# Optimization experiments

Measured on AMD Instinct MI355X. Metric: run time of the kernel, lower is better.

The kernel has to match this reference:

```python
import jax, jax.numpy as jnp
import numpy as np

# Intrinsics from innerProdLoss defaults
FX, FY, CX, CY = 48.0, 48.0, 48.0, 36.0
H, W = int(2 * CY), int(2 * CX)  # 72, 96
N = H * W                         # 6912 pixels
SIGMA2 = 1.0                      # geometric Gaussian-kernel bandwidth (reconstructed kern_mat)
EPS = 1e-8


def make_yz1_grid():
    # K = [[cx,fx,0],[cy,0,fy],[1,0,0]]; yz1_grid = inv(K) @ uv1_grid, shape [3, N]
    K = np.array([[CX, FX, 0.0], [CY, 0.0, FY], [1.0, 0.0, 0.0]], dtype=np.float64)
    invK = np.linalg.inv(K).astype(np.float32)
    u = np.arange(W, dtype=np.float32)
    v = np.arange(H, dtype=np.float32)
    uu = np.tile(u[None, :], (H, 1)).reshape(-1)
    vv = np.tile(v[:, None], (1, W)).reshape(-1)
    uv1 = np.stack([uu, vv, np.ones_like(uu)], axis=0)  # [3, N]
    return jnp.asarray(invK @ uv1)

YZ1 = make_yz1_grid()  # [3, N]


def kern_mat(p1, p2):
    # p1, p2: [B, 3, N] point clouds -> [B, N, N] Gaussian kernel exp(-||d||^2 / (2 sigma^2)).
    # Squared distances via norms + cross term (no [B,3,N,N] diff tensor).
    n1 = jnp.sum(p1 * p1, axis=1)                    # [B, N]
    n2 = jnp.sum(p2 * p2, axis=1)                    # [B, N]
    cross = jnp.einsum('bcm,bcn->bmn', p1, p2)       # [B, N, N]
    d2 = jnp.maximum(n1[:, :, None] + n2[:, None, :] - 2.0 * cross, 0.0)
    return jnp.exp(-d2 / (2.0 * SIGMA2))


def gramian(f1, f2):
    # f1, f2: [B, C, H, W] -> gramian [B, N, N] of L2-normalized features (norm_mode=1, kernalize=False).
    B, C, Hh, Ww = f1.shape
    n = Hh * Ww
    f1 = f1.reshape(B, C, n)
    f2 = f2.reshape(B, C, n)
    norm1 = jnp.linalg.norm(f1, axis=1)              # [B, N]
    norm2 = jnp.linalg.norm(f2, axis=1)
    fea_norm_sum = jnp.sum(norm1) + jnp.sum(norm2)
    f1n = f1 / (norm1[:, None, :] + EPS)
    f2n = f2 / (norm2[:, None, :] + EPS)
    gram = jnp.einsum('bcm,bcn->bmn', f1n, f2n) / n  # norm_mode=1 normalization
    return gram, fea_norm_sum


def setup_inputs() -> dict:
    key = jax.random.key(0)
    k1, k2, k3, k4, k5 = jax.random.split(key, 5)
    B, C = 1, 16
    feature1 = jax.random.normal(k1, (B, C, H, W), jnp.float32)
    feature2 = jax.random.normal(k2, (B, C, H, W), jnp.float32)
    depth1 = jax.random.uniform(k3, (B, 1, H, W), jnp.float32, 0.5, 5.0)
    depth2 = jax.random.uniform(k4, (B, 1, H, W), jnp.float32, 0.5, 5.0)
    pose1_2 = jnp.tile(jnp.eye(4, dtype=jnp.float32)[None], (B, 1, 1))
    pose_noise = jnp.eye(4, dtype=jnp.float32) + 0.01 * jax.random.normal(k5, (4, 4), jnp.float32)
    return {"feature1": feature1, "feature2": feature2, "depth1": depth1,
            "depth2": depth2, "pose1_2": pose1_2, "pose_noise": pose_noise}


def reference(feature1, feature2, depth1, depth2, pose1_2, pose_noise):
    B = depth1.shape[0]
    # gen_3D: back-project pixels using depth
    xyz1 = YZ1[None] * depth1.reshape(B, 1, N)       # [B, 3, N]
    xyz2 = YZ1[None] * depth2.reshape(B, 1, N)
    xyz2_homo = jnp.concatenate([xyz2, jnp.ones((B, 1, N), xyz2.dtype)], axis=1)  # [B, 4, N]
    xyz2_trans = jnp.matmul(pose1_2, xyz2_homo)[:, :3, :]

    gram_feat, fea_norm_sum = gramian(feature1, feature2)
    pcl_diff_exp = kern_mat(xyz1, xyz2_trans)

    # L2_norm=True, diff_mode=True -> scale by 100
    fea_norm_sum = fea_norm_sum * 100.0

    # diff_mode: noisy pose branch
    pose_noisy = jnp.matmul(pose1_2, pose_noise)
    xyz2_trans_noisy = jnp.matmul(pose_noisy, xyz2_homo)[:, :3, :]
    pcl_diff_exp_noisy = kern_mat(xyz1, xyz2_trans_noisy)

    inner_neg = -jnp.sum((pcl_diff_exp - pcl_diff_exp_noisy) * gram_feat)
    final_loss = inner_neg  # sparse_mode=False
    return final_loss, inner_neg, fea_norm_sum
```

## Files before the change

kernel.cpp:

```cpp
#include <hip/hip_runtime.h>
#include <math.h>

#define NPIX 6912
#define LOG2E 1.4426950408889634f

typedef __fp16 v8h  __attribute__((ext_vector_type(8)));
typedef float  v16f __attribute__((ext_vector_type(16)));

#define OFF_ROWFEAT 0
#define OFF_ROWGEO  221184
#define OFF_COLFEAT 442368
#define OFF_COLB1   663552
#define OFF_COLB2   884736
#define OFF_PART    1105920
#define OFF_NPART   1111104
#define NPART_BLOCKS 1296
#define NNORM_BLOCKS 108

__device__ __forceinline__ float fast_exp2(float x) { return __builtin_amdgcn_exp2f(x); }

__device__ __forceinline__ float wave_reduce_64(float v) {
    #pragma unroll
    for (int o = 32; o > 0; o >>= 1) v += __shfl_down(v, o, 64);
    return v;
}

__device__ __forceinline__ float block_reduce_256(float v, float* smem4) {
    __syncthreads();
    v = wave_reduce_64(v);
    const int lane = threadIdx.x & 63;
    const int w = threadIdx.x >> 6;
    if (lane == 0) smem4[w] = v;
    __syncthreads();
    float r = 0.0f;
    if (threadIdx.x == 0) r = smem4[0] + smem4[1] + smem4[2] + smem4[3];
    return r;
}

__device__ __forceinline__ void split_hl(float x, __fp16& h, __fp16& l) {
    h = (__fp16)x;
    l = (__fp16)(x - (float)h);
}

__global__ __launch_bounds__(64)
void preproc_kernel(const float* __restrict__ f1, const float* __restrict__ f2,
                    const float* __restrict__ d1, const float* __restrict__ d2,
                    const float* __restrict__ pose, const float* __restrict__ pnz,
                    char* __restrict__ wsb) {
    const int i = blockIdx.x * 64 + threadIdx.x;

    __fp16* rowfeat = (__fp16*)(wsb + OFF_ROWFEAT);
    __fp16* rowgeo  = (__fp16*)(wsb + OFF_ROWGEO);
    __fp16* colfeat = (__fp16*)(wsb + OFF_COLFEAT);
    __fp16* colB1   = (__fp16*)(wsb + OFF_COLB1);
    __fp16* colB2   = (__fp16*)(wsb + OFF_COLB2);
    float*  npart   = (float*)(wsb + OFF_NPART);

    float P[12];
    #pragma unroll
    for (int k = 0; k < 12; k++) P[k] = pose[k];
    float Q[12];
    #pragma unroll
    for (int r = 0; r < 3; r++) {
        #pragma unroll
        for (int c = 0; c < 4; c++) {
            float s = 0.0f;
            #pragma unroll
            for (int k = 0; k < 4; k++) s = fmaf(pose[r * 4 + k], pnz[k * 4 + c], s);
            Q[r * 4 + c] = s;
        }
    }

    const float inv48 = 1.0f / 48.0f;
    const int u = i % 96;
    const int v = i / 96;
    const float y1 = fmaf((float)u, inv48, -1.0f);
    const float y2 = fmaf((float)v, inv48, -0.75f);

    const float dep1 = d1[i];
    const float px = dep1, py = y1 * dep1, pz = y2 * dep1;
    const float n1 = px * px + py * py + pz * pz;
    const float wlog = -0.5f * LOG2E * n1;

    const float ptx = LOG2E * px, pty = LOG2E * py, ptz = LOG2E * pz;
    __fp16 phx, phy, phz, plx, ply, plz, wh, wl;
    split_hl(ptx, phx, plx);
    split_hl(pty, phy, ply);
    split_hl(ptz, phz, plz);
    split_hl(wlog, wh, wl);
    {
        __fp16 rg[16] = {phx, phy, phz,  phx, phy, phz,  plx, ply, plz,
                         (__fp16)1.0f, (__fp16)1.0f, wh, wl,
                         (__fp16)0, (__fp16)0, (__fp16)0};
        *(v8h*)(rowgeo + (size_t)i * 16)     = *(v8h*)(rg);
        *(v8h*)(rowgeo + (size_t)i * 16 + 8) = *(v8h*)(rg + 8);
    }

    const float dep2 = d2[i];
    const float a = dep2, b = y1 * dep2, g = y2 * dep2;
    const float t0 = P[0] * a + P[1] * b + P[2]  * g + P[3];
    const float t1 = P[4] * a + P[5] * b + P[6]  * g + P[7];
    const float t2 = P[8] * a + P[9] * b + P[10] * g + P[11];
    const float q0 = Q[0] * a + Q[1] * b + Q[2]  * g + Q[3];
    const float q1 = Q[4] * a + Q[5] * b + Q[6]  * g + Q[7];
    const float q2 = Q[8] * a + Q[9] * b + Q[10] * g + Q[11];
    const float nt = t0 * t0 + t1 * t1 + t2 * t2;
    const float nq = q0 * q0 + q1 * q1 + q2 * q2;
    const float cA = -0.5f * LOG2E * nt;
    const float cB = -0.5f * LOG2E * nq;

    __fp16 thx, thy, thz, tlx, tly, tlz, cAh, cAl;
    __fp16 qhx, qhy, qhz, qlx, qly, qlz, cBh, cBl;
    split_hl(t0, thx, tlx);
    split_hl(t1, thy, tly);
    split_hl(t2, thz, tlz);
    split_hl(cA, cAh, cAl);
    split_hl(q0, qhx, qlx);
    split_hl(q1, qhy, qly);
    split_hl(q2, qhz, qlz);
    split_hl(cB, cBh, cBl);
    {
        __fp16 b1a[16] = {thx, thy, thz,  tlx, tly, tlz,  thx, thy, thz,
                          cAh, cAl, (__fp16)1.0f, (__fp16)1.0f,
                          (__fp16)0, (__fp16)0, (__fp16)0};
        *(v8h*)(colB1 + (size_t)i * 16)     = *(v8h*)(b1a);
        *(v8h*)(colB1 + (size_t)i * 16 + 8) = *(v8h*)(b1a + 8);
    }
    {
        __fp16 b2a[16] = {qhx, qhy, qhz,  qlx, qly, qlz,  qhx, qhy, qhz,
                          cBh, cBl, (__fp16)1.0f, (__fp16)1.0f,
                          (__fp16)0, (__fp16)0, (__fp16)0};
        *(v8h*)(colB2 + (size_t)i * 16)     = *(v8h*)(b2a);
        *(v8h*)(colB2 + (size_t)i * 16 + 8) = *(v8h*)(b2a + 8);
    }

    float s1 = 0.0f, s2 = 0.0f;
    float v1[16], v2[16];
    #pragma unroll
    for (int cc = 0; cc < 16; cc++) {
        v1[cc] = f1[cc * NPIX + i];
        v2[cc] = f2[cc * NPIX + i];
        s1 = fmaf(v1[cc], v1[cc], s1);
        s2 = fmaf(v2[cc], v2[cc], s2);
    }
    const float nrm1 = sqrtf(s1), nrm2 = sqrtf(s2);
    const float r1 = 1.0f / (nrm1 + 1e-8f), r2 = 1.0f / (nrm2 + 1e-8f);
    {
        __fp16 rf[16], cf[16];
        #pragma unroll
        for (int cc = 0; cc < 16; cc++) {
            rf[cc] = (__fp16)(v1[cc] * r1);
            cf[cc] = (__fp16)(v2[cc] * r2);
        }
        *(v8h*)(rowfeat + (size_t)i * 16)     = *(v8h*)(rf);
        *(v8h*)(rowfeat + (size_t)i * 16 + 8) = *(v8h*)(rf + 8);
        *(v8h*)(colfeat + (size_t)i * 16)     = *(v8h*)(cf);
        *(v8h*)(colfeat + (size_t)i * 16 + 8) = *(v8h*)(cf + 8);
    }

    float tot = wave_reduce_64(nrm1 + nrm2);
    if (threadIdx.x == 0) npart[blockIdx.x] = tot;
}

__global__ __launch_bounds__(256)
void pair_kernel(const char* __restrict__ wsb) {
    __shared__ float smem4[4];

    const __fp16* rowfeat = (const __fp16*)(wsb + OFF_ROWFEAT);
    const __fp16* rowgeo  = (const __fp16*)(wsb + OFF_ROWGEO);
    const __fp16* colfeat = (const __fp16*)(wsb + OFF_COLFEAT);
    const __fp16* colB1   = (const __fp16*)(wsb + OFF_COLB1);
    const __fp16* colB2   = (const __fp16*)(wsb + OFF_COLB2);
    float*        part    = (float*)(const_cast<char*>(wsb) + OFF_PART);

    const int t = threadIdx.x;
    const int w = t >> 6;
    const int L = t & 63;
    const int c31 = L & 31;
    const int kh8 = (L >> 5) * 8;

    const int arow = blockIdx.y * 128 + w * 32 + c31;
    const v8h afeat = *(const v8h*)(rowfeat + (size_t)arow * 16 + kh8);
    const v8h ageo  = *(const v8h*)(rowgeo  + (size_t)arow * 16 + kh8);

    const int cbase = blockIdx.x * 288;
    const size_t boff0 = (size_t)(cbase + c31) * 16 + kh8;

    float acc0 = 0.0f, acc1 = 0.0f;

    v8h BF[3], B1[3], B2[3];
    #pragma unroll
    for (int s = 0; s < 2; s++) {
        const size_t o = boff0 + (size_t)s * 32 * 16;
        BF[s] = *(const v8h*)(colfeat + o);
        B1[s] = *(const v8h*)(colB1   + o);
        B2[s] = *(const v8h*)(colB2   + o);
    }

    #pragma unroll
    for (int ct = 0; ct < 9; ct++) {
        const int cur = ct % 3;
        if (ct < 7) {
            const int nxt = (ct + 2) % 3;
            const size_t o = boff0 + (size_t)(ct + 2) * 32 * 16;
            BF[nxt] = *(const v8h*)(colfeat + o);
            B1[nxt] = *(const v8h*)(colB1   + o);
            B2[nxt] = *(const v8h*)(colB2   + o);
        }

        v16f z = {};
        const v16f dotv = __builtin_amdgcn_mfma_f32_32x32x16_f16(afeat, BF[cur], z, 0, 0, 0);
        const v16f a1v  = __builtin_amdgcn_mfma_f32_32x32x16_f16(ageo,  B1[cur], z, 0, 0, 0);
        const v16f a2v  = __builtin_amdgcn_mfma_f32_32x32x16_f16(ageo,  B2[cur], z, 0, 0, 0);

        #pragma unroll
        for (int i = 0; i < 8; i++) {
            const float e1a = fast_exp2(a1v[i]);
            const float e2a = fast_exp2(a2v[i]);
            const float e1b = fast_exp2(a1v[i + 8]);
            const float e2b = fast_exp2(a2v[i + 8]);
            acc0 = fmaf(e1a - e2a, dotv[i], acc0);
            acc1 = fmaf(e1b - e2b, dotv[i + 8], acc1);
        }
    }

    float v = wave_reduce_64(acc0 + acc1);
    if (L == 0) smem4[w] = v;
    __syncthreads();
    if (t == 0)
        part[blockIdx.y * 24 + blockIdx.x] = smem4[0] + smem4[1] + smem4[2] + smem4[3];
}

__global__ __launch_bounds__(256)
void finalize_kernel(const char* __restrict__ wsb, float* __restrict__ out) {
    __shared__ float smem4[4];
    const float* part  = (const float*)(wsb + OFF_PART);
    const float* npart = (const float*)(wsb + OFF_NPART);
    const int t = threadIdx.x;

    float s = 0.0f;
    for (int i = t; i < NPART_BLOCKS; i += 256) s += part[i];
    const float tot = block_reduce_256(s, smem4);

    float ns = (t < NNORM_BLOCKS) ? npart[t] : 0.0f;
    const float ntot = block_reduce_256(ns, smem4);

    if (t == 0) {
        const float vc = -tot * (1.0f / (float)NPIX);
        out[0] = vc;
        out[1] = vc;
        out[2] = 100.0f * ntot;
    }
}

extern "C" void kernel_launch(void* const* d_in, const int* in_sizes, int n_in,
                              void* d_out, int out_size, void* d_ws, size_t ws_size,
                              hipStream_t stream) {
    const float* feature1 = (const float*)d_in[0];
    const float* feature2 = (const float*)d_in[1];
    const float* depth1   = (const float*)d_in[2];
    const float* depth2   = (const float*)d_in[3];
    const float* pose1_2  = (const float*)d_in[4];
    const float* posenz   = (const float*)d_in[5];
    float* out = (float*)d_out;
    char*  wsb = (char*)d_ws;

    preproc_kernel<<<108, 64, 0, stream>>>(feature1, feature2, depth1, depth2,
                                           pose1_2, posenz, wsb);
    dim3 grid(24, 54);
    pair_kernel<<<grid, 256, 0, stream>>>(wsb);
    finalize_kernel<<<1, 256, 0, stream>>>(wsb, out);
}
```

Measured before the change: 85.85 us.

## Stage column operands in LDS shared across waves with double buffering

In the old code each of the four waves loaded its own copy of the column operand tiles from global memory. Now the block loads each column tile once into a double-buffered LDS staging area and all four waves read it from there, cutting redundant global loads. The column tile per block shrinks from 288 to 256 columns and the grid grows to 27x54, with the partial-sum buffer offsets adjusted to match. The cost is block-wide barriers on every stage and extra LDS traffic.

```diff
diff --git a/kernel.cpp b/kernel.cpp
--- a/kernel.cpp
+++ b/kernel.cpp
@@ -13,8 +13,8 @@
 #define OFF_COLB1   663552
 #define OFF_COLB2   884736
 #define OFF_PART    1105920
-#define OFF_NPART   1111104
-#define NPART_BLOCKS 1296
+#define OFF_NPART   1111752
+#define NPART_BLOCKS 1458
 #define NNORM_BLOCKS 108
 
 __device__ __forceinline__ float fast_exp2(float x) { return __builtin_amdgcn_exp2f(x); }
@@ -164,6 +164,7 @@
 
 __global__ __launch_bounds__(256)
 void pair_kernel(const char* __restrict__ wsb) {
+    __shared__ __align__(16) __fp16 sbuf[2][3][128 * 8];
     __shared__ float smem4[4];
 
     const __fp16* rowfeat = (const __fp16*)(wsb + OFF_ROWFEAT);
@@ -183,44 +184,56 @@
     const v8h afeat = *(const v8h*)(rowfeat + (size_t)arow * 16 + kh8);
     const v8h ageo  = *(const v8h*)(rowgeo  + (size_t)arow * 16 + kh8);
 
-    const int cbase = blockIdx.x * 288;
-    const size_t boff0 = (size_t)(cbase + c31) * 16 + kh8;
+    const int cbase = blockIdx.x * 256;
+
+    auto stage = [&](int b, int st) {
+        const int colbase = cbase + st * 64;
+        #pragma unroll
+        for (int jj = 0; jj < 2; jj++) {
+            const int j = t + jj * 256;
+            if (j < 384) {
+                const int a = j >> 7;
+                const int r = j & 127;
+                const int s = r >> 6;
+                const int h = (r >> 5) & 1;
+                const int c = s * 32 + (r & 31);
+                const __fp16* src = (a == 0 ? colfeat : (a == 1 ? colB1 : colB2));
+                *(v8h*)(&sbuf[b][a][r * 8]) =
+                    *(const v8h*)(src + (size_t)(colbase + c) * 16 + h * 8);
+            }
+        }
+    };
 
     float acc0 = 0.0f, acc1 = 0.0f;
-
-    v8h BF[3], B1[3], B2[3];
-    #pragma unroll
-    for (int s = 0; s < 2; s++) {
-        const size_t o = boff0 + (size_t)s * 32 * 16;
-        BF[s] = *(const v8h*)(colfeat + o);
-        B1[s] = *(const v8h*)(colB1   + o);
-        B2[s] = *(const v8h*)(colB2   + o);
-    }
-
-    #pragma unroll
-    for (int ct = 0; ct < 9; ct++) {
-        const int cur = ct % 3;
-        if (ct < 7) {
-            const int nxt = (ct + 2) % 3;
-            const size_t o = boff0 + (size_t)(ct + 2) * 32 * 16;
-            BF[nxt] = *(const v8h*)(colfeat + o);
-            B1[nxt] = *(const v8h*)(colB1   + o);
-            B2[nxt] = *(const v8h*)(colB2   + o);
-        }
-
-        v16f z = {};
-        const v16f dotv = __builtin_amdgcn_mfma_f32_32x32x16_f16(afeat, BF[cur], z, 0, 0, 0);
-        const v16f a1v  = __builtin_amdgcn_mfma_f32_32x32x16_f16(ageo,  B1[cur], z, 0, 0, 0);
-        const v16f a2v  = __builtin_amdgcn_mfma_f32_32x32x16_f16(ageo,  B2[cur], z, 0, 0, 0);
-
-        #pragma unroll
-        for (int i = 0; i < 8; i++) {
-            const float e1a = fast_exp2(a1v[i]);
-            const float e2a = fast_exp2(a2v[i]);
-            const float e1b = fast_exp2(a1v[i + 8]);
-            const float e2b = fast_exp2(a2v[i + 8]);
-            acc0 = fmaf(e1a - e2a, dotv[i], acc0);
-            acc1 = fmaf(e1b - e2b, dotv[i + 8], acc1);
+    stage(0, 0);
+
+    #pragma unroll
+    for (int st = 0; st < 4; st++) {
+        const int cur = st & 1;
+        __syncthreads();
+        if (st < 3) stage(1 - cur, st + 1);
+
+        #pragma unroll
+        for (int s = 0; s < 2; s++) {
+            const int g = s * 64 + (L >> 5) * 32 + c31;
+            const v8h bf = *(const v8h*)(&sbuf[cur][0][g * 8]);
+            const v8h b1 = *(const v8h*)(&sbuf[cur][1][g * 8]);
+            const v8h b2 = *(const v8h*)(&sbuf[cur][2][g * 8]);
+
+            v16f z = {};
+            const v16f dotv = __builtin_amdgcn_mfma_f32_32x32x16_f16(afeat, bf, z, 0, 0, 0);
+            const v16f a1v  = __builtin_amdgcn_mfma_f32_32x32x16_f16(ageo,  b1, z, 0, 0, 0);
+            const v16f a2v  = __builtin_amdgcn_mfma_f32_32x32x16_f16(ageo,  b2, z, 0, 0, 0);
+
+            #pragma unroll
+            for (int i = 0; i < 8; i++) {
+                const float e1a = fast_exp2(a1v[i]);
+                const float e2a = fast_exp2(a2v[i]);
+                const float e1b = fast_exp2(a1v[i + 8]);
+                const float e2b = fast_exp2(a2v[i + 8]);
+                acc0 = fmaf(e1a - e2a, dotv[i], acc0);
+                acc1 = fmaf(e1b - e2b, dotv[i + 8], acc1);
+            }
         }
     }
 
@@ -228,7 +241,7 @@
     if (L == 0) smem4[w] = v;
     __syncthreads();
     if (t == 0)
-        part[blockIdx.y * 24 + blockIdx.x] = smem4[0] + smem4[1] + smem4[2] + smem4[3];
+        part[blockIdx.y * 27 + blockIdx.x] = smem4[0] + smem4[1] + smem4[2] + smem4[3];
 }
 
 __global__ __launch_bounds__(256)
@@ -267,7 +280,7 @@
 
     preproc_kernel<<<108, 64, 0, stream>>>(feature1, feature2, depth1, depth2,
                                            pose1_2, posenz, wsb);
-    dim3 grid(24, 54);
+    dim3 grid(27, 54);
     pair_kernel<<<grid, 256, 0, stream>>>(wsb);
     finalize_kernel<<<1, 256, 0, stream>>>(wsb, out);
 }
```

Result: slower. 93.70 us (+9.1%).
